# Performance work log

Hardware: AMD Instinct MI355X
Metric: run time of the kernel (lower is better)

Reference implementation:

```python
import jax, jax.numpy as jnp
import numpy as np

V, E, H, L, C, B, S = 50000, 300, 512, 2, 25, 64, 256
FORGET_BIAS = 1.0  # tf.contrib.rnn.LSTMCell default


def setup_inputs() -> dict:
    key = jax.random.key(0)
    ks = jax.random.split(key, 16)
    std = 0.01  # truncated_normal stddev in weight_and_bias
    inp = {
        "input_ids": jax.random.randint(ks[0], (B, S), 0, V, dtype=jnp.int32),
        "lengths": jax.random.randint(ks[1], (B,), 1, S + 1, dtype=jnp.int32),
        "emb": jax.random.normal(ks[2], (V, E), dtype=jnp.float32) * 0.05,
    }
    in_dims = [E] + [2 * H] * (L - 1)
    i = 3
    for l, d in enumerate(in_dims):
        for dirn in ("fw", "bw"):
            inp[f"w_{dirn}{l}"] = jax.random.normal(ks[i], (d + H, 4 * H), dtype=jnp.float32) * std
            inp[f"b_{dirn}{l}"] = jnp.zeros((4 * H,), dtype=jnp.float32)
            i += 1
    inp["wd"] = jax.random.normal(ks[i], (2 * H, C), dtype=jnp.float32) * std
    inp["bd"] = jnp.full((C,), 0.1, dtype=jnp.float32)
    return inp


def lstm_layer(x, w, b, lengths):
    """x: [S, B, D] time-major. Returns [S, B, H]. TF LSTMCell gate order i,j,f,o."""
    Bn = x.shape[1]
    Hn = b.shape[0] // 4
    c0 = jnp.zeros((Bn, Hn), x.dtype)
    h0 = jnp.zeros((Bn, Hn), x.dtype)

    def step(carry, xt_t):
        xt, t = xt_t
        c, h = carry
        g = jnp.concatenate([xt, h], axis=-1) @ w + b  # [B, 4H]
        i_, j_, f_, o_ = jnp.split(g, 4, axis=-1)
        cn = jax.nn.sigmoid(f_ + FORGET_BIAS) * c + jax.nn.sigmoid(i_) * jnp.tanh(j_)
        hn = jax.nn.sigmoid(o_) * jnp.tanh(cn)
        m = (t < lengths)[:, None]
        # past sequence_length: state frozen, output zero (TF rnn semantics)
        c2 = jnp.where(m, cn, c)
        h2 = jnp.where(m, hn, h)
        hout = jnp.where(m, hn, jnp.zeros_like(hn))
        return (c2, h2), hout

    ts = jnp.arange(x.shape[0])
    _, hs = jax.lax.scan(step, (c0, h0), (x, ts))
    return hs


def reverse_seq(x, lengths):
    """Reverse the first `lengths[b]` steps of x[b] (TF _reverse_seq). x: [B, S, D]."""
    Sn = x.shape[1]
    t = jnp.arange(Sn)[None, :]
    idx = jnp.where(t < lengths[:, None], lengths[:, None] - 1 - t, t)
    return jnp.take_along_axis(x, idx[:, :, None], axis=1)


def reference(input_ids, lengths, emb, w_fw0, b_fw0, w_bw0, b_bw0,
              w_fw1, b_fw1, w_bw1, b_bw1, wd, bd):
    x = emb[input_ids]  # [B, S, E]
    layers = [(w_fw0, b_fw0, w_bw0, b_bw0), (w_fw1, b_fw1, w_bw1, b_bw1)]
    h = x
    for wf, bf, wb, bb in layers:
        fw = jnp.swapaxes(lstm_layer(jnp.swapaxes(h, 0, 1), wf, bf, lengths), 0, 1)
        hr = reverse_seq(h, lengths)
        bw = jnp.swapaxes(lstm_layer(jnp.swapaxes(hr, 0, 1), wb, bb, lengths), 0, 1)
        bw = reverse_seq(bw, lengths)
        h = jnp.concatenate([fw, bw], axis=-1)  # [B, S, 2H]
    logits = h @ wd + bd  # [B, S, C]
    return jax.nn.softmax(logits, axis=-1)
```

## Files before the change

kernel.cpp:

```cpp
#include <hip/hip_runtime.h>
#include <hip/hip_bf16.h>

#define S_LEN 256
#define BATCH 64
#define EMB   300
#define EPAD  320
#define HID   512
#define G4H   2048
#define NCLS  25
#define TWOH  1024

using bf16 = __hip_bfloat16;
typedef short bf8v __attribute__((ext_vector_type(8)));
typedef float f32x4 __attribute__((ext_vector_type(4)));
typedef unsigned long long ull;

__device__ __forceinline__ float us2f(unsigned short u) {
    union { unsigned int i; float f; } v; v.i = ((unsigned int)u) << 16; return v.f;
}
__device__ __forceinline__ unsigned short f2us(float f) {
    union { bf16 v; unsigned short s; } cv; cv.v = __float2bfloat16(f); return cv.s;
}
__device__ __forceinline__ float sigm(float x) { return 1.f / (1.f + __expf(-x)); }

__global__ void embed_kernel(const int* __restrict__ ids,
                             const float* __restrict__ emb,
                             bf16* __restrict__ x)
{
    int r = blockIdx.x;
    int t = r >> 6, b = r & 63;
    int id = ids[b * S_LEN + t];
    const float* src = emb + (size_t)id * EMB;
    bf16* dst = x + (size_t)r * EPAD;
    for (int e = threadIdx.x; e < EPAD; e += blockDim.x) {
        float v = (e < EMB) ? src[e] : 0.f;
        dst[e] = __float2bfloat16(v);
    }
}

__global__ void wtrans_kernel(const float* __restrict__ w_fw0, const float* __restrict__ w_bw0,
                              const float* __restrict__ w_fw1, const float* __restrict__ w_bw1,
                              bf16* __restrict__ whTb)
{
    __shared__ float tile[32][33];
    int wl = blockIdx.z;
    const float* W; int D;
    if (wl == 0)      { W = w_fw0; D = EMB; }
    else if (wl == 1) { W = w_bw0; D = EMB; }
    else if (wl == 2) { W = w_fw1; D = TWOH; }
    else              { W = w_bw1; D = TWOH; }
    int k0 = blockIdx.x * 32, n0 = blockIdx.y * 32;
    int tx = threadIdx.x, ty = threadIdx.y;
    tile[ty][tx] = W[(size_t)(D + k0 + ty) * G4H + n0 + tx];
    __syncthreads();
    int k = k0 + tx;
    int n = n0 + ty;
    int u = n & 511, g = n >> 9;
    whTb[(((size_t)wl * 512 + u) * 4 + g) * 512 + k] = __float2bfloat16(tile[tx][ty]);
}

__global__ void wxtrans_kernel(const float* __restrict__ w_fw0, const float* __restrict__ w_bw0,
                               const float* __restrict__ w_fw1, const float* __restrict__ w_bw1,
                               bf16* __restrict__ wxTb)
{
    __shared__ float tile[32][33];
    int wl = blockIdx.z;
    const float* W; int D;
    if (wl == 0)      { W = w_fw0; D = EMB; }
    else if (wl == 1) { W = w_bw0; D = EMB; }
    else if (wl == 2) { W = w_fw1; D = TWOH; }
    else              { W = w_bw1; D = TWOH; }
    int k0 = blockIdx.x * 32, n0 = blockIdx.y * 32;
    int tx = threadIdx.x, ty = threadIdx.y;
    float v = (k0 + ty < D) ? W[(size_t)(k0 + ty) * G4H + n0 + tx] : 0.f;
    tile[ty][tx] = v;
    __syncthreads();
    int n = n0 + ty;
    int u = n & 511, g = n >> 9;
    wxTb[((size_t)wl * G4H + (u * 4 + g)) * 1024 + k0 + tx] = __float2bfloat16(tile[tx][ty]);
}

__global__ __launch_bounds__(512)
void gates_mfma(const bf16* __restrict__ A, int strideA, int K,
                const bf16* __restrict__ wxTb,
                const float* __restrict__ b_fw, const float* __restrict__ b_bw,
                const int* __restrict__ lengths,
                bf16* __restrict__ G4)
{
    const int z  = blockIdx.z;
    const int m0 = blockIdx.x * 256;
    const int n0 = blockIdx.y * 128;
    const int tid = threadIdx.x;
    const float* bias = z ? b_bw : b_fw;

    __shared__ __align__(16) unsigned short smem[24576];
    unsigned short* As = smem;
    unsigned short* Bs = smem + 16384;

    const int ca = tid & 7;
    const bf16* srcA[4];
    const bf16* srcB[2];
    int lofsA[4], lofsB[2];
#pragma unroll
    for (int j = 0; j < 4; ++j) {
        int row = j * 64 + (tid >> 3);
        int r = m0 + row, t = r >> 6, b = r & 63;
        int st = t;
        if (z) { int len = lengths[b]; st = (t < len) ? (len - 1 - t) : t; }
        srcA[j] = A + (size_t)(st * 64 + b) * strideA + ca * 8;
        lofsA[j] = row * 64 + ((ca ^ (row & 7)) << 3);
    }
#pragma unroll
    for (int j = 0; j < 2; ++j) {
        int row = j * 64 + (tid >> 3);
        srcB[j] = wxTb + ((size_t)z * G4H + n0 + row) * 1024 + ca * 8;
        lofsB[j] = row * 64 + ((ca ^ (row & 7)) << 3);
    }

    const int l = tid & 63, lo16 = l & 15, hi4 = l >> 4;
    const int wv = tid >> 6, wm = wv >> 1, wn = wv & 1;

    f32x4 acc[4][4];
#pragma unroll
    for (int mi = 0; mi < 4; ++mi)
#pragma unroll
        for (int ni = 0; ni < 4; ++ni)
#pragma unroll
            for (int rr = 0; rr < 4; ++rr) acc[mi][ni][rr] = 0.f;

    uint4 ra[4], rb[2];
#pragma unroll
    for (int j = 0; j < 4; ++j) ra[j] = *reinterpret_cast<const uint4*>(srcA[j]);
#pragma unroll
    for (int j = 0; j < 2; ++j) rb[j] = *reinterpret_cast<const uint4*>(srcB[j]);

    const int nk = K >> 6;
    for (int kt = 0; kt < nk; ++kt) {
        __syncthreads();
#pragma unroll
        for (int j = 0; j < 4; ++j) *reinterpret_cast<uint4*>(&As[lofsA[j]]) = ra[j];
#pragma unroll
        for (int j = 0; j < 2; ++j) *reinterpret_cast<uint4*>(&Bs[lofsB[j]]) = rb[j];
        __syncthreads();
        if (kt + 1 < nk) {
#pragma unroll
            for (int j = 0; j < 4; ++j) {
                srcA[j] += 64;
                ra[j] = *reinterpret_cast<const uint4*>(srcA[j]);
            }
#pragma unroll
            for (int j = 0; j < 2; ++j) {
                srcB[j] += 64;
                rb[j] = *reinterpret_cast<const uint4*>(srcB[j]);
            }
        }
#pragma unroll
        for (int ks = 0; ks < 2; ++ks) {
            bf8v af[4], bfv[4];
#pragma unroll
            for (int mi = 0; mi < 4; ++mi) {
                int row = wm * 64 + mi * 16 + lo16;
                int c = ks * 4 + hi4;
                af[mi] = *reinterpret_cast<const bf8v*>(&As[row * 64 + ((c ^ (row & 7)) << 3)]);
            }
#pragma unroll
            for (int ni = 0; ni < 4; ++ni) {
                int row = wn * 64 + ni * 16 + lo16;
                int c = ks * 4 + hi4;
                bfv[ni] = *reinterpret_cast<const bf8v*>(&Bs[row * 64 + ((c ^ (row & 7)) << 3)]);
            }
#pragma unroll
            for (int mi = 0; mi < 4; ++mi)
#pragma unroll
                for (int ni = 0; ni < 4; ++ni)
                    acc[mi][ni] = __builtin_amdgcn_mfma_f32_16x16x32_bf16(
                        af[mi], bfv[ni], acc[mi][ni], 0, 0, 0);
        }
    }

    float bv[4];
#pragma unroll
    for (int ni = 0; ni < 4; ++ni) {
        int np = n0 + wn * 64 + ni * 16 + lo16;
        int raw = (np & 3) * 512 + (np >> 2);
        bv[ni] = bias[raw];
    }
#pragma unroll
    for (int h = 0; h < 2; ++h) {
        __syncthreads();
        if ((wm >> 1) == h) {
#pragma unroll
            for (int mi = 0; mi < 4; ++mi)
#pragma unroll
                for (int ni = 0; ni < 4; ++ni)
#pragma unroll
                    for (int rr = 0; rr < 4; ++rr) {
                        int m = (wm & 1) * 64 + mi * 16 + hi4 * 4 + rr;
                        int n = wn * 64 + ni * 16 + lo16;
                        smem[m * 132 + n] = f2us(acc[mi][ni][rr] + bv[ni]);
                    }
        }
        __syncthreads();
        {
            int row = tid >> 2;
            int cs  = (tid & 3) * 32;
            int m = m0 + h * 128 + row;
            int tt = m >> 6, b = m & 63;
            const unsigned short* src = smem + row * 132 + cs;
            bf16* gout = G4 + (((size_t)z * S_LEN + tt) * 64 + b) * G4H + n0 + cs;
#pragma unroll
            for (int j = 0; j < 8; ++j)
                *reinterpret_cast<ull*>(gout + j * 4) =
                    *reinterpret_cast<const ull*>(src + j * 4);
        }
    }
}

__global__ __launch_bounds__(512, 1)
void lstm_seq(const bf16* __restrict__ G4, const bf16* __restrict__ whTb,
              const int* __restrict__ lengths, unsigned short* __restrict__ hbuf,
              unsigned int* __restrict__ flags, bf16* __restrict__ hcat)
{
    __shared__ __align__(16) unsigned short hl[32 * 512];
    __shared__ __align__(16) unsigned short hout[32 * 64];

    const int bx = blockIdx.x;
    const int d  = bx >> 4;
    const int bh = (bx >> 3) & 1;
    const int cg = bx & 7;
    const int tid = threadIdx.x;
    const int w = tid >> 6, l = tid & 63;
    const int lo16 = l & 15, hi4 = l >> 4;
    const int u0 = cg * 64 + w * 8;

    bf8v afr[2][16];
#pragma unroll
    for (int mt = 0; mt < 2; ++mt) {
        const bf16* wr = whTb + (((size_t)d * 512 + u0 + mt * 4 + (lo16 >> 2)) * 4
                                 + (lo16 & 3)) * 512 + hi4 * 8;
#pragma unroll
        for (int kt = 0; kt < 16; ++kt)
            afr[mt][kt] = *reinterpret_cast<const bf8v*>(wr + kt * 32);
    }

    int len_[2];
    float c_st[2][2], h_st[2][2];
#pragma unroll
    for (int nt = 0; nt < 2; ++nt) {
        len_[nt] = lengths[bh * 32 + nt * 16 + lo16];
#pragma unroll
        for (int mt = 0; mt < 2; ++mt) { c_st[mt][nt] = 0.f; h_st[mt][nt] = 0.f; }
    }

    for (int t = 0; t < S_LEN; ++t) {
        ull gv[2][2];
#pragma unroll
        for (int mt = 0; mt < 2; ++mt)
#pragma unroll
            for (int nt = 0; nt < 2; ++nt) {
                int b = bh * 32 + nt * 16 + lo16;
                int u = u0 + mt * 4 + hi4;
                gv[mt][nt] = *reinterpret_cast<const ull*>(
                    G4 + (((size_t)(d * S_LEN + t)) * 64 + b) * G4H + u * 4);
            }

        if (t > 0 && tid < 8) {
            const unsigned int* fb = flags + (size_t)(t - 1) * 32 + (d * 2 + bh) * 8;
            while (__hip_atomic_load(fb + tid, __ATOMIC_RELAXED,
                                     __HIP_MEMORY_SCOPE_AGENT) == 0u)
                __builtin_amdgcn_s_sleep(2);
        }
        __syncthreads();

        const ull* hsrc = reinterpret_cast<const ull*>(
            hbuf + ((size_t)((t & 1) * 2 + d) * 64 + bh * 32) * 512);
        ull pv[8];
#pragma unroll
        for (int i = 0; i < 8; ++i)
            pv[i] = __hip_atomic_load(hsrc + i * 512 + tid,
                                      __ATOMIC_RELAXED, __HIP_MEMORY_SCOPE_AGENT);
#pragma unroll
        for (int i = 0; i < 8; ++i) {
            int wd_ = i * 512 + tid;
            int bl = wd_ >> 7, r = wd_ & 127;
            int c = r >> 1, half = r & 1;
            *reinterpret_cast<ull*>(&hl[bl * 512 + ((c ^ (bl & 7)) << 3) + (half << 2)]) = pv[i];
        }
        __syncthreads();

        f32x4 acc[2][2];
#pragma unroll
        for (int mt = 0; mt < 2; ++mt)
#pragma unroll
            for (int nt = 0; nt < 2; ++nt) {
                const unsigned short* gs = reinterpret_cast<const unsigned short*>(&gv[mt][nt]);
                f32x4 av;
#pragma unroll
                for (int g = 0; g < 4; ++g) av[g] = us2f(gs[g]);
                acc[mt][nt] = av;
            }

#pragma unroll
        for (int kt = 0; kt < 16; ++kt) {
            bf8v bfv[2];
#pragma unroll
            for (int nt = 0; nt < 2; ++nt) {
                int bl = nt * 16 + lo16;
                int c  = kt * 4 + hi4;
                bfv[nt] = *reinterpret_cast<const bf8v*>(
                    &hl[bl * 512 + ((c ^ (bl & 7)) << 3)]);
            }
#pragma unroll
            for (int mt = 0; mt < 2; ++mt)
#pragma unroll
                for (int nt = 0; nt < 2; ++nt)
                    acc[mt][nt] = __builtin_amdgcn_mfma_f32_16x16x32_bf16(
                        afr[mt][kt], bfv[nt], acc[mt][nt], 0, 0, 0);
        }

#pragma unroll
        for (int mt = 0; mt < 2; ++mt)
#pragma unroll
            for (int nt = 0; nt < 2; ++nt) {
                bool msk = (t < len_[nt]);
                float i_ = sigm(acc[mt][nt][0]);
                float j_ = tanhf(acc[mt][nt][1]);
                float f_ = sigm(acc[mt][nt][2] + 1.0f);
                float o_ = sigm(acc[mt][nt][3]);
                float cn = f_ * c_st[mt][nt] + i_ * j_;
                float hn = o_ * tanhf(cn);
                if (msk) c_st[mt][nt] = cn;
                h_st[mt][nt] = msk ? hn : h_st[mt][nt];
                hout[(nt * 16 + lo16) * 64 + w * 8 + mt * 4 + hi4] = f2us(h_st[mt][nt]);
            }
        __syncthreads();

        {
            int bl = tid >> 4, uq = (tid & 15) * 4;
            ull v = *reinterpret_cast<const ull*>(&hout[bl * 64 + uq]);
            unsigned short* hdst = hbuf + ((size_t)(((t + 1) & 1) * 2 + d) * 64
                                           + bh * 32 + bl) * 512 + cg * 64 + uq;
            __hip_atomic_store(reinterpret_cast<ull*>(hdst), v,
                               __ATOMIC_RELAXED, __HIP_MEMORY_SCOPE_AGENT);
        }
        asm volatile("s_waitcnt vmcnt(0)" ::: "memory");
        __syncthreads();
        if (tid == 0)
            __hip_atomic_store(&flags[(size_t)t * 32 + (d * 2 + bh) * 8 + cg], 1u,
                               __ATOMIC_RELAXED, __HIP_MEMORY_SCOPE_AGENT);

#pragma unroll
        for (int mt = 0; mt < 2; ++mt)
#pragma unroll
            for (int nt = 0; nt < 2; ++nt) {
                int b = bh * 32 + nt * 16 + lo16;
                int u = u0 + mt * 4 + hi4;
                bool msk = (t < len_[nt]);
                int p = (d == 1 && msk) ? (len_[nt] - 1 - t) : t;
                hcat[((size_t)p * 64 + b) * TWOH + (size_t)d * 512 + u] =
                    __float2bfloat16(msk ? h_st[mt][nt] : 0.f);
            }
    }
}

__global__ __launch_bounds__(256)
void dense_softmax(const bf16* __restrict__ h, const float* __restrict__ wd,
                   const float* __restrict__ bd, float* __restrict__ out)
{
    __shared__ __align__(16) bf16 wdT[NCLS][1032];
    for (int i = threadIdx.x; i < TWOH * NCLS; i += 256) {
        int k = i / NCLS, c = i % NCLS;
        wdT[c][k] = __float2bfloat16(wd[i]);
    }
    __syncthreads();
    const int c  = threadIdx.x & 31;
    const int rl = threadIdx.x >> 5;
#pragma unroll 1
    for (int pass = 0; pass < 8; ++pass) {
        int r = blockIdx.x * 64 + pass * 8 + rl;
        const bf16* hrow = h + (size_t)r * TWOH;
        float acc = -1e30f;
        if (c < NCLS) {
            acc = 0.f;
            for (int k = 0; k < TWOH; k += 8) {
                uint4 hv = *reinterpret_cast<const uint4*>(hrow + k);
                uint4 wv = *reinterpret_cast<const uint4*>(&wdT[c][k]);
                const unsigned short* hs  = reinterpret_cast<const unsigned short*>(&hv);
                const unsigned short* wsp = reinterpret_cast<const unsigned short*>(&wv);
#pragma unroll
                for (int j = 0; j < 8; ++j) acc += us2f(hs[j]) * us2f(wsp[j]);
            }
            acc += bd[c];
        }
        float mx = acc;
#pragma unroll
        for (int o = 16; o; o >>= 1) mx = fmaxf(mx, __shfl_xor(mx, o, 32));
        float e = (c < NCLS) ? __expf(acc - mx) : 0.f;
        float sm = e;
#pragma unroll
        for (int o = 16; o; o >>= 1) sm += __shfl_xor(sm, o, 32);
        if (c < NCLS) {
            int s = r >> 6, b = r & 63;
            out[((size_t)b * S_LEN + s) * NCLS + c] = e / sm;
        }
    }
}

extern "C" void kernel_launch(void* const* d_in, const int* in_sizes, int n_in,
                              void* d_out, int out_size, void* d_ws, size_t ws_size,
                              hipStream_t stream)
{
    const int*   ids   = (const int*)  d_in[0];
    const int*   lens  = (const int*)  d_in[1];
    const float* emb   = (const float*)d_in[2];
    const float* w_fw0 = (const float*)d_in[3];
    const float* b_fw0 = (const float*)d_in[4];
    const float* w_bw0 = (const float*)d_in[5];
    const float* b_bw0 = (const float*)d_in[6];
    const float* w_fw1 = (const float*)d_in[7];
    const float* b_fw1 = (const float*)d_in[8];
    const float* w_bw1 = (const float*)d_in[9];
    const float* b_bw1 = (const float*)d_in[10];
    const float* wd    = (const float*)d_in[11];
    const float* bd    = (const float*)d_in[12];
    float* out = (float*)d_out;

    char* ws = (char*)d_ws;
    size_t off = 0;
    auto alloc = [&](size_t bytes) {
        void* p = ws + off;
        off += (bytes + 255) & ~(size_t)255;
        return p;
    };
    bf16*  x      = (bf16*) alloc((size_t)S_LEN * BATCH * EPAD * 2);
    bf16*  G4     = (bf16*) alloc((size_t)2 * S_LEN * BATCH * G4H * 2);
    bf16*  hcat0  = (bf16*) alloc((size_t)S_LEN * BATCH * TWOH * 2);
    bf16*  hcat1  = (bf16*) alloc((size_t)S_LEN * BATCH * TWOH * 2);
    bf16*  whTb   = (bf16*) alloc((size_t)4 * 512 * 4 * 512 * 2);
    bf16*  wxTb   = (bf16*) alloc((size_t)4 * G4H * 1024 * 2);
    unsigned short* hbuf = (unsigned short*)alloc((size_t)2 * 2 * BATCH * HID * 2);
    unsigned int* flags  = (unsigned int*) alloc((size_t)2 * S_LEN * 32 * 4);

    embed_kernel<<<S_LEN * BATCH, 128, 0, stream>>>(ids, emb, x);
    wtrans_kernel<<<dim3(16, 64, 4), dim3(32, 32), 0, stream>>>(w_fw0, w_bw0, w_fw1, w_bw1, whTb);
    wxtrans_kernel<<<dim3(32, 64, 4), dim3(32, 32), 0, stream>>>(w_fw0, w_bw0, w_fw1, w_bw1, wxTb);
    hipMemsetAsync(flags, 0, (size_t)2 * S_LEN * 32 * 4, stream);

    for (int layer = 0; layer < 2; ++layer) {
        hipMemsetAsync(hbuf, 0, (size_t)2 * 2 * BATCH * HID * 2, stream);
        const bf16* Ain   = layer ? hcat0 : x;
        int strideA       = layer ? TWOH : EPAD;
        int K             = layer ? 1024 : EPAD;
        const float* bfp  = layer ? b_fw1 : b_fw0;
        const float* bbp  = layer ? b_bw1 : b_bw0;
        bf16* hcat        = layer ? hcat1 : hcat0;

        gates_mfma<<<dim3(64, 16, 2), 512, 0, stream>>>(
            Ain, strideA, K, wxTb + (size_t)layer * 2 * G4H * 1024,
            bfp, bbp, lens, G4);

        const bf16*  Gp   = G4;
        const bf16*  whp  = whTb + (size_t)layer * 2 * 512 * 4 * 512;
        const int*   lnp  = lens;
        unsigned short* hbp = hbuf;
        unsigned int* flp = flags + (size_t)layer * S_LEN * 32;
        bf16*        hcp  = hcat;
        void* args[6] = { &Gp, &whp, &lnp, &hbp, &flp, &hcp };
        hipLaunchCooperativeKernel(lstm_seq, dim3(32), dim3(512), args, 0, stream);
    }
    dense_softmax<<<256, 256, 0, stream>>>(hcat1, wd, bd, out);

    (void)in_sizes; (void)n_in; (void)out_size; (void)ws_size;
}
```

Measured before the change: 3.587 ms.

## Replace flag-based step barrier with sentinel-filled per-step hidden state buffer

The recurrent kernel no longer waits on per-block flags and no longer does a barrier, vmcnt wait and flag store after each step. Each timestep's hidden state now goes to its own slot in a sequence buffer pre-filled with 0xFFFF. Readers poll directly on the data until no sentinel remains, which removes one sync round-trip per step. The buffer is shared with the transposed input weights, which are now transposed per layer just before use. The risk is that a bf16 value of 0xFFFF (a NaN) would stall the poll, and per-lane 8-byte atomicity of the data has to hold.

```diff
diff --git a/kernel.cpp b/kernel.cpp
--- a/kernel.cpp
+++ b/kernel.cpp
@@ -59,17 +59,12 @@
     whTb[(((size_t)wl * 512 + u) * 4 + g) * 512 + k] = __float2bfloat16(tile[tx][ty]);
 }
 
-__global__ void wxtrans_kernel(const float* __restrict__ w_fw0, const float* __restrict__ w_bw0,
-                               const float* __restrict__ w_fw1, const float* __restrict__ w_bw1,
-                               bf16* __restrict__ wxTb)
+__global__ void wxtrans_kernel(const float* __restrict__ w_fw, const float* __restrict__ w_bw,
+                               int D, bf16* __restrict__ wxTb)
 {
     __shared__ float tile[32][33];
-    int wl = blockIdx.z;
-    const float* W; int D;
-    if (wl == 0)      { W = w_fw0; D = EMB; }
-    else if (wl == 1) { W = w_bw0; D = EMB; }
-    else if (wl == 2) { W = w_fw1; D = TWOH; }
-    else              { W = w_bw1; D = TWOH; }
+    int z = blockIdx.z;
+    const float* W = z ? w_bw : w_fw;
     int k0 = blockIdx.x * 32, n0 = blockIdx.y * 32;
     int tx = threadIdx.x, ty = threadIdx.y;
     float v = (k0 + ty < D) ? W[(size_t)(k0 + ty) * G4H + n0 + tx] : 0.f;
@@ -77,7 +72,7 @@
     __syncthreads();
     int n = n0 + ty;
     int u = n & 511, g = n >> 9;
-    wxTb[((size_t)wl * G4H + (u * 4 + g)) * 1024 + k0 + tx] = __float2bfloat16(tile[tx][ty]);
+    wxTb[((size_t)z * G4H + (u * 4 + g)) * 1024 + k0 + tx] = __float2bfloat16(tile[tx][ty]);
 }
 
 __global__ __launch_bounds__(512)
@@ -218,8 +213,8 @@
 
 __global__ __launch_bounds__(512, 1)
 void lstm_seq(const bf16* __restrict__ G4, const bf16* __restrict__ whTb,
-              const int* __restrict__ lengths, unsigned short* __restrict__ hbuf,
-              unsigned int* __restrict__ flags, bf16* __restrict__ hcat)
+              const int* __restrict__ lengths, unsigned short* __restrict__ hseq,
+              bf16* __restrict__ hcat)
 {
     __shared__ __align__(16) unsigned short hl[32 * 512];
     __shared__ __align__(16) unsigned short hout[32 * 64];
@@ -264,21 +259,22 @@
                     G4 + (((size_t)(d * S_LEN + t)) * 64 + b) * G4H + u * 4);
             }
 
-        if (t > 0 && tid < 8) {
-            const unsigned int* fb = flags + (size_t)(t - 1) * 32 + (d * 2 + bh) * 8;
-            while (__hip_atomic_load(fb + tid, __ATOMIC_RELAXED,
-                                     __HIP_MEMORY_SCOPE_AGENT) == 0u)
-                __builtin_amdgcn_s_sleep(2);
-        }
-        __syncthreads();
-
         const ull* hsrc = reinterpret_cast<const ull*>(
-            hbuf + ((size_t)((t & 1) * 2 + d) * 64 + bh * 32) * 512);
+            hseq + ((size_t)(t * 2 + d) * 64 + bh * 32) * 512);
         ull pv[8];
 #pragma unroll
         for (int i = 0; i < 8; ++i)
             pv[i] = __hip_atomic_load(hsrc + i * 512 + tid,
                                       __ATOMIC_RELAXED, __HIP_MEMORY_SCOPE_AGENT);
+#pragma unroll
+        for (int i = 0; i < 8; ++i) {
+            while (__builtin_expect((pv[i] & 0xFFFFull) == 0xFFFFull, 0)) {
+                __builtin_amdgcn_s_sleep(1);
+                pv[i] = __hip_atomic_load(hsrc + i * 512 + tid,
+                                          __ATOMIC_RELAXED, __HIP_MEMORY_SCOPE_AGENT);
+            }
+        }
+
 #pragma unroll
         for (int i = 0; i < 8; ++i) {
             int wd_ = i * 512 + tid;
@@ -338,16 +334,11 @@
         {
             int bl = tid >> 4, uq = (tid & 15) * 4;
             ull v = *reinterpret_cast<const ull*>(&hout[bl * 64 + uq]);
-            unsigned short* hdst = hbuf + ((size_t)(((t + 1) & 1) * 2 + d) * 64
+            unsigned short* hdst = hseq + ((size_t)((t + 1) * 2 + d) * 64
                                            + bh * 32 + bl) * 512 + cg * 64 + uq;
             __hip_atomic_store(reinterpret_cast<ull*>(hdst), v,
                                __ATOMIC_RELAXED, __HIP_MEMORY_SCOPE_AGENT);
         }
-        asm volatile("s_waitcnt vmcnt(0)" ::: "memory");
-        __syncthreads();
-        if (tid == 0)
-            __hip_atomic_store(&flags[(size_t)t * 32 + (d * 2 + bh) * 8 + cg], 1u,
-                               __ATOMIC_RELAXED, __HIP_MEMORY_SCOPE_AGENT);
 
 #pragma unroll
         for (int mt = 0; mt < 2; ++mt)
@@ -432,40 +423,41 @@
         off += (bytes + 255) & ~(size_t)255;
         return p;
     };
+    const size_t hseq_bytes = (size_t)(S_LEN + 1) * 2 * BATCH * HID * 2;
     bf16*  x      = (bf16*) alloc((size_t)S_LEN * BATCH * EPAD * 2);
     bf16*  G4     = (bf16*) alloc((size_t)2 * S_LEN * BATCH * G4H * 2);
     bf16*  hcat0  = (bf16*) alloc((size_t)S_LEN * BATCH * TWOH * 2);
     bf16*  hcat1  = (bf16*) alloc((size_t)S_LEN * BATCH * TWOH * 2);
     bf16*  whTb   = (bf16*) alloc((size_t)4 * 512 * 4 * 512 * 2);
-    bf16*  wxTb   = (bf16*) alloc((size_t)4 * G4H * 1024 * 2);
-    unsigned short* hbuf = (unsigned short*)alloc((size_t)2 * 2 * BATCH * HID * 2);
-    unsigned int* flags  = (unsigned int*) alloc((size_t)2 * S_LEN * 32 * 4);
+    void*  scratch = alloc(hseq_bytes);
 
     embed_kernel<<<S_LEN * BATCH, 128, 0, stream>>>(ids, emb, x);
     wtrans_kernel<<<dim3(16, 64, 4), dim3(32, 32), 0, stream>>>(w_fw0, w_bw0, w_fw1, w_bw1, whTb);
-    wxtrans_kernel<<<dim3(32, 64, 4), dim3(32, 32), 0, stream>>>(w_fw0, w_bw0, w_fw1, w_bw1, wxTb);
-    hipMemsetAsync(flags, 0, (size_t)2 * S_LEN * 32 * 4, stream);
 
     for (int layer = 0; layer < 2; ++layer) {
-        hipMemsetAsync(hbuf, 0, (size_t)2 * 2 * BATCH * HID * 2, stream);
         const bf16* Ain   = layer ? hcat0 : x;
         int strideA       = layer ? TWOH : EPAD;
         int K             = layer ? 1024 : EPAD;
+        const float* Wf   = layer ? w_fw1 : w_fw0;
+        const float* Wb   = layer ? w_bw1 : w_bw0;
+        int D             = layer ? TWOH : EMB;
         const float* bfp  = layer ? b_fw1 : b_fw0;
         const float* bbp  = layer ? b_bw1 : b_bw0;
         bf16* hcat        = layer ? hcat1 : hcat0;
 
+        wxtrans_kernel<<<dim3(32, 64, 2), dim3(32, 32), 0, stream>>>(Wf, Wb, D, (bf16*)scratch);
         gates_mfma<<<dim3(64, 16, 2), 512, 0, stream>>>(
-            Ain, strideA, K, wxTb + (size_t)layer * 2 * G4H * 1024,
-            bfp, bbp, lens, G4);
+            Ain, strideA, K, (const bf16*)scratch, bfp, bbp, lens, G4);
+
+        hipMemsetAsync(scratch, 0xFF, hseq_bytes, stream);
+        hipMemsetAsync(scratch, 0x00, (size_t)2 * BATCH * HID * 2, stream);
 
         const bf16*  Gp   = G4;
         const bf16*  whp  = whTb + (size_t)layer * 2 * 512 * 4 * 512;
         const int*   lnp  = lens;
-        unsigned short* hbp = hbuf;
-        unsigned int* flp = flags + (size_t)layer * S_LEN * 32;
+        unsigned short* hsp = (unsigned short*)scratch;
         bf16*        hcp  = hcat;
-        void* args[6] = { &Gp, &whp, &lnp, &hbp, &flp, &hcp };
+        void* args[5] = { &Gp, &whp, &lnp, &hsp, &hcp };
         hipLaunchCooperativeKernel(lstm_seq, dim3(32), dim3(512), args, 0, stream);
     }
     dense_softmax<<<256, 256, 0, stream>>>(hcat1, wd, bd, out);
```

Result: no change. 3.574 ms (-0.4%).
